# Optimization experiments

Measured on AMD Instinct MI355X. Metric: run time of the kernel, lower is better.

Reference implementation:

```python
import jax, jax.numpy as jnp
import numpy as np

N_NODES = 50000
N_EDGES = 1600000
IN_DIM = 64
HEADS = 8
DHEAD = 8  # out_dim per head
CLAMP = 5.0


def _xavier(key, shape):
    # xavier_normal_ for a torch Linear weight [out, in]; we store transposed [in, out]
    fan_in, fan_out = shape[0], shape[1]
    std = np.sqrt(2.0 / (fan_in + fan_out))
    return jax.random.normal(key, shape, jnp.float32) * jnp.float32(std)


def setup_inputs() -> dict:
    key = jax.random.key(0)
    ks = jax.random.split(key, 8)
    x = jax.random.normal(ks[0], (N_NODES, IN_DIM), jnp.float32)
    edge_attr = jax.random.normal(ks[1], (N_EDGES, IN_DIM), jnp.float32)
    edge_index = jax.random.randint(ks[2], (2, N_EDGES), 0, N_NODES)
    HD = HEADS * DHEAD
    WQ = _xavier(ks[3], (IN_DIM, HD)); bQ = jnp.zeros((HD,), jnp.float32)
    WK = _xavier(ks[4], (IN_DIM, HD))  # use_bias=False -> no bias for K
    WV = _xavier(ks[5], (IN_DIM, HD))  # no bias for V
    WE1 = _xavier(ks[6], (IN_DIM, HD)); bE1 = jnp.zeros((HD,), jnp.float32)
    return {"x": x, "edge_attr": edge_attr, "WQ": WQ, "bQ": bQ, "WK": WK,
            "WV": WV, "WE1": WE1, "bE1": bE1, "edge_index": edge_index}


def _segment_softmax(s, seg, num_segments):
    # pyg_softmax: numerically-stable softmax over edges grouped by destination node
    m = jax.ops.segment_max(s, seg, num_segments=num_segments)
    m = jnp.where(jnp.isfinite(m), m, jnp.float32(0.0))  # empty segments -> 0
    e = jnp.exp(s - m[seg])
    den = jax.ops.segment_sum(e, seg, num_segments=num_segments)
    return e / (den[seg] + jnp.float32(1e-16))


def _forward(x, edge_attr, WQ, bQ, WK, WV, WE1, bE1, edge_index):
    Q = (x @ WQ + bQ).reshape(N_NODES, HEADS, DHEAD)
    K = (x @ WK).reshape(N_NODES, HEADS, DHEAD)
    V = (x @ WV).reshape(N_NODES, HEADS, DHEAD)
    E = (edge_attr @ WE1 + bE1).reshape(N_EDGES, HEADS, DHEAD)
    src, dst = edge_index[0], edge_index[1]
    # score = K[src] * Q[dst]; score_e = score * E  (attn_product='mul', act=Identity)
    score_e = K[src] * Q[dst] * E                  # [Ne, H, D]
    wE = score_e.reshape(N_EDGES, HEADS * DHEAD)   # edge output
    s = score_e.sum(-1, keepdims=True) / jnp.sqrt(jnp.float32(DHEAD))  # [Ne, H, 1]
    s = jnp.clip(s, -CLAMP, CLAMP)
    alpha = _segment_softmax(s, dst, N_NODES)      # [Ne, H, 1]
    msg = V[src] * alpha
    wV = jax.ops.segment_sum(msg, dst, num_segments=N_NODES)
    # edge_enhance (edge_reweight=False): add segment-sum of score_e * alpha
    wV = wV + jax.ops.segment_sum(score_e * alpha, dst, num_segments=N_NODES)
    return wV, wE


def reference(x, edge_attr, WQ, bQ, WK, WV, WE1, bE1, edge_index):
    return _forward(x, edge_attr, WQ, bQ, WK, WV, WE1, bE1, edge_index)
```

## Files before the change

### kernel.cpp

```cpp
#include <hip/hip_runtime.h>

#define NN 50000
#define NE 1600000
#define CLAMP_V 5.0f
#define NB 2048
#define CH ((NE + NB - 1) / NB)
#define BSHIFT 9
#define NBUCK ((NN + (1 << BSHIFT) - 1) >> BSHIFT)
#define BPAD 128

typedef __attribute__((ext_vector_type(4))) short bf16x4;
typedef __attribute__((ext_vector_type(4))) float f32x4;

static __device__ __forceinline__ short f2bf(float x) {
    unsigned u = __builtin_bit_cast(unsigned, x);
    u += 0x7FFF + ((u >> 16) & 1);
    return (short)(u >> 16);
}

__global__ __launch_bounds__(256) void proj_kernel(
    const float* __restrict__ x,
    const float* __restrict__ WQ, const float* __restrict__ bQ,
    const float* __restrict__ WK, const float* __restrict__ WVw,
    float* __restrict__ Q, float* __restrict__ K, float* __restrict__ V)
{
    __shared__ float sWQ[4096], sWK[4096], sWV[4096];
    for (int i = threadIdx.x; i < 4096; i += 256) {
        sWQ[i] = WQ[i]; sWK[i] = WK[i]; sWV[i] = WVw[i];
    }
    __syncthreads();
    const int col = threadIdx.x & 63;
    const int nl  = threadIdx.x >> 6;
    const float bq = bQ[col];
    for (int node = blockIdx.x * 4 + nl; node < NN; node += gridDim.x * 4) {
        const float* xr = x + (size_t)node * 64;
        float aq = 0.f, ak = 0.f, av = 0.f;
        #pragma unroll
        for (int j = 0; j < 64; ++j) {
            float xv = xr[j];
            aq = fmaf(xv, sWQ[j*64+col], aq);
            ak = fmaf(xv, sWK[j*64+col], ak);
            av = fmaf(xv, sWV[j*64+col], av);
        }
        Q[(size_t)node*64+col] = aq + bq;
        K[(size_t)node*64+col] = ak;
        V[(size_t)node*64+col] = av;
    }
}

__global__ __launch_bounds__(256) void hist1_kernel(
    const int* __restrict__ ei, int* __restrict__ blockHist)
{
    __shared__ int h[BPAD];
    if (threadIdx.x < BPAD) h[threadIdx.x] = 0;
    __syncthreads();
    const int b  = blockIdx.x;
    const int e0 = b * CH;
    const int e1 = (e0 + CH < NE) ? e0 + CH : NE;
    for (int e = e0 + threadIdx.x; e < e1; e += 256)
        atomicAdd(&h[ei[NE + e] >> BSHIFT], 1);
    __syncthreads();
    if (threadIdx.x < NBUCK) blockHist[b * BPAD + threadIdx.x] = h[threadIdx.x];
}

__global__ __launch_bounds__(64) void scanA_kernel(
    int* __restrict__ blockHist, int* __restrict__ bucketTotal)
{
    const int k    = blockIdx.x;
    const int lane = threadIdx.x;
    int running = 0;
    for (int c = 0; c < NB; c += 64) {
        int v = blockHist[(c + lane) * BPAD + k];
        int incl = v;
        #pragma unroll
        for (int d = 1; d < 64; d <<= 1) {
            int t = __shfl_up(incl, d);
            if (lane >= d) incl += t;
        }
        blockHist[(c + lane) * BPAD + k] = running + (incl - v);
        running += __shfl(incl, 63);
    }
    if (lane == 0) bucketTotal[k] = running;
}

__global__ void scanB_kernel(const int* __restrict__ bucketTotal,
                             int* __restrict__ bucketStart)
{
    int acc = 0;
    for (int k = 0; k < NBUCK; ++k) { bucketStart[k] = acc; acc += bucketTotal[k]; }
    bucketStart[NBUCK] = acc;
}

__global__ __launch_bounds__(256) void scatter1_kernel(
    const int* __restrict__ ei, const int* __restrict__ blockHist,
    const int* __restrict__ bucketStart, uint2* __restrict__ binned)
{
    __shared__ int cur[BPAD];
    const int b = blockIdx.x;
    if (threadIdx.x < NBUCK)
        cur[threadIdx.x] = bucketStart[threadIdx.x] + blockHist[b * BPAD + threadIdx.x];
    __syncthreads();
    const int e0 = b * CH;
    const int e1 = (e0 + CH < NE) ? e0 + CH : NE;
    for (int e = e0 + threadIdx.x; e < e1; e += 256) {
        const unsigned src = ei[e], dst = ei[NE + e];
        const int pos = atomicAdd(&cur[dst >> BSHIFT], 1);
        binned[pos] = make_uint2((dst << 16) | src, (unsigned)e);
    }
}

__global__ __launch_bounds__(1024) void sort2_kernel(
    const uint2* __restrict__ binned, const int* __restrict__ bucketStart,
    uint2* __restrict__ sorted)
{
    __shared__ int cnt[512];
    __shared__ int pre[512];
    const int b  = blockIdx.x;
    const int lo = bucketStart[b];
    const int hi = bucketStart[b + 1];
    if (threadIdx.x < 512) cnt[threadIdx.x] = 0;
    __syncthreads();
    for (int p = lo + threadIdx.x; p < hi; p += 1024)
        atomicAdd(&cnt[(binned[p].x >> 16) & 511], 1);
    __syncthreads();
    if (threadIdx.x < 512) pre[threadIdx.x] = cnt[threadIdx.x];
    __syncthreads();
    for (int d = 1; d < 512; d <<= 1) {
        int t = (threadIdx.x < 512 && threadIdx.x >= d) ? pre[threadIdx.x - d] : 0;
        __syncthreads();
        if (threadIdx.x < 512) pre[threadIdx.x] += t;
        __syncthreads();
    }
    if (threadIdx.x < 512)
        cnt[threadIdx.x] = lo + pre[threadIdx.x] - cnt[threadIdx.x];
    __syncthreads();
    for (int p = lo + threadIdx.x; p < hi; p += 1024) {
        const uint2 q = binned[p];
        const int pos = atomicAdd(&cnt[(q.x >> 16) & 511], 1);
        sorted[pos] = q;
    }
}

__global__ __launch_bounds__(256) void edge_fused_kernel(
    const float* __restrict__ edge_attr,
    const float* __restrict__ WE1, const float* __restrict__ bE1,
    const uint2* __restrict__ sorted,
    const float* __restrict__ Q, const float* __restrict__ K,
    const float* __restrict__ V,
    float* __restrict__ wE, float* __restrict__ den, float* __restrict__ Num)
{
    __shared__ float Elds[4][16 * 64];
    __shared__ float exL[4][16 * 8];
    __shared__ int   dstL[4][16];
    const int tid  = threadIdx.x;
    const int wv   = tid >> 6;
    const int lane = tid & 63;
    const int g    = lane >> 4;
    const int rowl = lane & 15;

    bf16x4 bF[4][4];
    float  bias[4];
    #pragma unroll
    for (int cb = 0; cb < 4; ++cb) {
        const int col = rowl + 16 * cb;
        bias[cb] = bE1[col];
        #pragma unroll
        for (int ks = 0; ks < 4; ++ks) {
            bf16x4 t;
            #pragma unroll
            for (int j = 0; j < 4; ++j)
                t[j] = f2bf(WE1[(ks * 16 + g * 4 + j) * 64 + col]);
            bF[cb][ks] = t;
        }
    }

    const float inv_sqrt8 = 0.35355339059327373f;

    for (int tile = blockIdx.x; tile < (NE / 64); tile += gridDim.x) {
        const int pBase = tile * 64 + wv * 16;

        const uint2 qv  = sorted[pBase + rowl];
        const int  srcv = qv.x & 0xffff;
        const int  dstv = qv.x >> 16;
        const int  eidv = (int)qv.y;
        if (lane < 16) dstL[wv][lane] = dstv;

        bf16x4 aF[4];
        const float* ar = edge_attr + (size_t)eidv * 64 + g * 4;
        #pragma unroll
        for (int ks = 0; ks < 4; ++ks) {
            f32x4 v = __builtin_nontemporal_load(
                reinterpret_cast<const f32x4*>(ar + ks * 16));
            bf16x4 t;
            #pragma unroll
            for (int j = 0; j < 4; ++j) t[j] = f2bf(v[j]);
            aF[ks] = t;
        }

        f32x4 acc[4];
        #pragma unroll
        for (int cb = 0; cb < 4; ++cb) {
            acc[cb][0] = bias[cb]; acc[cb][1] = bias[cb];
            acc[cb][2] = bias[cb]; acc[cb][3] = bias[cb];
        }
        #pragma unroll
        for (int cb = 0; cb < 4; ++cb)
            #pragma unroll
            for (int ks = 0; ks < 4; ++ks)
                acc[cb] = __builtin_amdgcn_mfma_f32_16x16x16bf16_1k(
                    aF[ks], bF[cb][ks], acc[cb], 0, 0, 0);

        #pragma unroll
        for (int cb = 0; cb < 4; ++cb)
            #pragma unroll
            for (int r = 0; r < 4; ++r)
                Elds[wv][(g * 4 + r) * 64 + rowl + 16 * cb] = acc[cb][r];

        #pragma unroll
        for (int qi = 0; qi < 4; ++qi) {
            const int el  = qi * 4 + g;
            const int eid = __shfl(eidv, el);
            const int src = __shfl(srcv, el);
            const int dst = __shfl(dstv, el);
            const f32x4 Kv = *reinterpret_cast<const f32x4*>(K + (size_t)src * 64 + rowl * 4);
            const f32x4 Qv = *reinterpret_cast<const f32x4*>(Q + (size_t)dst * 64 + rowl * 4);
            const f32x4 Vv = *reinterpret_cast<const f32x4*>(V + (size_t)src * 64 + rowl * 4);
            f32x4* eslot = reinterpret_cast<f32x4*>(&Elds[wv][el * 64 + rowl * 4]);
            const f32x4 El = *eslot;
            f32x4 sc;
            #pragma unroll
            for (int j = 0; j < 4; ++j) sc[j] = Kv[j] * Qv[j] * El[j];
            __builtin_nontemporal_store(sc,
                reinterpret_cast<f32x4*>(wE + (size_t)eid * 64 + rowl * 4));
            float ss = sc[0] + sc[1] + sc[2] + sc[3];
            ss += __shfl_xor(ss, 1);
            float s = fminf(fmaxf(ss * inv_sqrt8, -CLAMP_V), CLAMP_V);
            float ex = __expf(s);
            if ((rowl & 1) == 0)
                exL[wv][el * 8 + (rowl >> 1)] = ex;
            f32x4 t;
            #pragma unroll
            for (int j = 0; j < 4; ++j) t[j] = ex * (Vv[j] + sc[j]);
            *eslot = t;
        }

        float accP = 0.f, accD = 0.f;
        int cur = dstL[wv][0];
        #pragma unroll
        for (int el = 0; el < 16; ++el) {
            accP += Elds[wv][el * 64 + lane];
            accD += exL[wv][el * 8 + (lane & 7)];
            const int nxt = (el < 15) ? dstL[wv][el + 1] : -1;
            if (nxt != cur) {
                atomicAdd(&Num[(size_t)cur * 64 + lane], accP);
                if (lane < 8) atomicAdd(&den[cur * 8 + lane], accD);
                accP = 0.f; accD = 0.f; cur = nxt;
            }
        }
    }
}

__global__ __launch_bounds__(256) void finalize_kernel(
    const float* __restrict__ Num, const float* __restrict__ den,
    float* __restrict__ wV)
{
    const int i = blockIdx.x * 256 + threadIdx.x;
    if (i >= NN * 16) return;
    const int c4 = i & 15;
    const int n  = i >> 4;
    const int h  = c4 >> 1;
    const float d = den[n * 8 + h] + 1e-16f;
    f32x4 v = reinterpret_cast<const f32x4*>(Num)[i];
    v[0] /= d; v[1] /= d; v[2] /= d; v[3] /= d;
    reinterpret_cast<f32x4*>(wV)[i] = v;
}

extern "C" void kernel_launch(void* const* d_in, const int* in_sizes, int n_in,
                              void* d_out, int out_size, void* d_ws, size_t ws_size,
                              hipStream_t stream) {
    const float* x         = (const float*)d_in[0];
    const float* edge_attr = (const float*)d_in[1];
    const float* WQ        = (const float*)d_in[2];
    const float* bQ        = (const float*)d_in[3];
    const float* WK        = (const float*)d_in[4];
    const float* WVw       = (const float*)d_in[5];
    const float* WE1       = (const float*)d_in[6];
    const float* bE1       = (const float*)d_in[7];
    const int*   ei        = (const int*)d_in[8];

    float* out = (float*)d_out;
    float* wV = out;
    float* wE = out + (size_t)NN * 64;

    float* Q           = (float*)d_ws;
    float* K           = Q + (size_t)NN * 64;
    float* V           = K + (size_t)NN * 64;
    float* den         = V + (size_t)NN * 64;
    float* Num         = den + (size_t)NN * 8;
    int*   blockHist   = (int*)(Num + (size_t)NN * 64);
    int*   bucketTotal = blockHist + NB * BPAD;
    int*   bucketStart = bucketTotal + BPAD;
    uint2* binned      = (uint2*)(bucketStart + BPAD);
    uint2* sorted      = binned + NE;

    hipMemsetAsync(den, 0, (size_t)NN * (8 + 64) * sizeof(float), stream);

    hist1_kernel<<<NB, 256, 0, stream>>>(ei, blockHist);
    scanA_kernel<<<NBUCK, 64, 0, stream>>>(blockHist, bucketTotal);
    scanB_kernel<<<1, 1, 0, stream>>>(bucketTotal, bucketStart);
    scatter1_kernel<<<NB, 256, 0, stream>>>(ei, blockHist, bucketStart, binned);
    sort2_kernel<<<NBUCK, 1024, 0, stream>>>(binned, bucketStart, sorted);
    proj_kernel<<<1024, 256, 0, stream>>>(x, WQ, bQ, WK, WVw, Q, K, V);
    edge_fused_kernel<<<2048, 256, 0, stream>>>(edge_attr, WE1, bE1, sorted,
                                                Q, K, V, wE, den, Num);
    finalize_kernel<<<(NN * 16 + 255) / 256, 256, 0, stream>>>(Num, den, wV);
}
```

Baseline: 354.5 us.

## Fuse histogram with projection, parallelize bucket scan, pad edge LDS, double edge grid

The histogram and node-projection kernels are merged into one launch, with block ranges split by blockIdx, which removes a launch and lets the two independent phases overlap. The single-thread bucket scan becomes a 64-lane wavefront shuffle scan. The edge kernel's LDS tile stride is padded from 64 to 68 to reduce bank conflicts, and its grid is doubled to 4096 blocks. The fused kernel always allocates 48KB of LDS even for histogram blocks, which may limit occupancy for that phase.

Result: slower. 402.1 us (+13.4%).

```diff
diff --git a/kernel.cpp b/kernel.cpp
--- a/kernel.cpp
+++ b/kernel.cpp
@@ -8,6 +8,8 @@
 #define BSHIFT 9
 #define NBUCK ((NN + (1 << BSHIFT) - 1) >> BSHIFT)
 #define BPAD 128
+#define PROJ_BLOCKS 1024
+#define ESTR 68
 
 typedef __attribute__((ext_vector_type(4))) short bf16x4;
 typedef __attribute__((ext_vector_type(4))) float f32x4;
@@ -18,13 +20,30 @@
     return (short)(u >> 16);
 }
 
-__global__ __launch_bounds__(256) void proj_kernel(
+__global__ __launch_bounds__(256) void histproj_kernel(
+    const int* __restrict__ ei, int* __restrict__ blockHist,
     const float* __restrict__ x,
     const float* __restrict__ WQ, const float* __restrict__ bQ,
     const float* __restrict__ WK, const float* __restrict__ WVw,
     float* __restrict__ Q, float* __restrict__ K, float* __restrict__ V)
 {
-    __shared__ float sWQ[4096], sWK[4096], sWV[4096];
+    __shared__ float sW[3 * 4096];
+    if (blockIdx.x < NB) {
+        int* h = (int*)sW;
+        if (threadIdx.x < BPAD) h[threadIdx.x] = 0;
+        __syncthreads();
+        const int b  = blockIdx.x;
+        const int e0 = b * CH;
+        const int e1 = (e0 + CH < NE) ? e0 + CH : NE;
+        for (int e = e0 + threadIdx.x; e < e1; e += 256)
+            atomicAdd(&h[ei[NE + e] >> BSHIFT], 1);
+        __syncthreads();
+        if (threadIdx.x < NBUCK) blockHist[b * BPAD + threadIdx.x] = h[threadIdx.x];
+        return;
+    }
+    float* sWQ = sW;
+    float* sWK = sW + 4096;
+    float* sWV = sW + 8192;
     for (int i = threadIdx.x; i < 4096; i += 256) {
         sWQ[i] = WQ[i]; sWK[i] = WK[i]; sWV[i] = WVw[i];
     }
@@ -32,7 +51,8 @@
     const int col = threadIdx.x & 63;
     const int nl  = threadIdx.x >> 6;
     const float bq = bQ[col];
-    for (int node = blockIdx.x * 4 + nl; node < NN; node += gridDim.x * 4) {
+    const int pb  = blockIdx.x - NB;
+    for (int node = pb * 4 + nl; node < NN; node += PROJ_BLOCKS * 4) {
         const float* xr = x + (size_t)node * 64;
         float aq = 0.f, ak = 0.f, av = 0.f;
         #pragma unroll
@@ -46,21 +66,6 @@
         K[(size_t)node*64+col] = ak;
         V[(size_t)node*64+col] = av;
     }
-}
-
-__global__ __launch_bounds__(256) void hist1_kernel(
-    const int* __restrict__ ei, int* __restrict__ blockHist)
-{
-    __shared__ int h[BPAD];
-    if (threadIdx.x < BPAD) h[threadIdx.x] = 0;
-    __syncthreads();
-    const int b  = blockIdx.x;
-    const int e0 = b * CH;
-    const int e1 = (e0 + CH < NE) ? e0 + CH : NE;
-    for (int e = e0 + threadIdx.x; e < e1; e += 256)
-        atomicAdd(&h[ei[NE + e] >> BSHIFT], 1);
-    __syncthreads();
-    if (threadIdx.x < NBUCK) blockHist[b * BPAD + threadIdx.x] = h[threadIdx.x];
 }
 
 __global__ __launch_bounds__(64) void scanA_kernel(
@@ -83,12 +88,23 @@
     if (lane == 0) bucketTotal[k] = running;
 }
 
-__global__ void scanB_kernel(const int* __restrict__ bucketTotal,
-                             int* __restrict__ bucketStart)
-{
-    int acc = 0;
-    for (int k = 0; k < NBUCK; ++k) { bucketStart[k] = acc; acc += bucketTotal[k]; }
-    bucketStart[NBUCK] = acc;
+__global__ __launch_bounds__(64) void scanB_kernel(
+    const int* __restrict__ bucketTotal, int* __restrict__ bucketStart)
+{
+    const int lane = threadIdx.x;
+    int carry = 0;
+    for (int base = 0; base <= NBUCK; base += 64) {
+        const int idx = base + lane;
+        int v = (idx < NBUCK) ? bucketTotal[idx] : 0;
+        int incl = v;
+        #pragma unroll
+        for (int d = 1; d < 64; d <<= 1) {
+            int t = __shfl_up(incl, d);
+            if (lane >= d) incl += t;
+        }
+        if (idx <= NBUCK) bucketStart[idx] = carry + incl - v;
+        carry += __shfl(incl, 63);
+    }
 }
 
 __global__ __launch_bounds__(256) void scatter1_kernel(
@@ -149,7 +165,7 @@
     const float* __restrict__ V,
     float* __restrict__ wE, float* __restrict__ den, float* __restrict__ Num)
 {
-    __shared__ float Elds[4][16 * 64];
+    __shared__ float Elds[4][16 * ESTR];
     __shared__ float exL[4][16 * 8];
     __shared__ int   dstL[4][16];
     const int tid  = threadIdx.x;
@@ -214,7 +230,7 @@
         for (int cb = 0; cb < 4; ++cb)
             #pragma unroll
             for (int r = 0; r < 4; ++r)
-                Elds[wv][(g * 4 + r) * 64 + rowl + 16 * cb] = acc[cb][r];
+                Elds[wv][(g * 4 + r) * ESTR + rowl + 16 * cb] = acc[cb][r];
 
         #pragma unroll
         for (int qi = 0; qi < 4; ++qi) {
@@ -225,7 +241,7 @@
             const f32x4 Kv = *reinterpret_cast<const f32x4*>(K + (size_t)src * 64 + rowl * 4);
             const f32x4 Qv = *reinterpret_cast<const f32x4*>(Q + (size_t)dst * 64 + rowl * 4);
             const f32x4 Vv = *reinterpret_cast<const f32x4*>(V + (size_t)src * 64 + rowl * 4);
-            f32x4* eslot = reinterpret_cast<f32x4*>(&Elds[wv][el * 64 + rowl * 4]);
+            f32x4* eslot = reinterpret_cast<f32x4*>(&Elds[wv][el * ESTR + rowl * 4]);
             const f32x4 El = *eslot;
             f32x4 sc;
             #pragma unroll
@@ -248,7 +264,7 @@
         int cur = dstL[wv][0];
         #pragma unroll
         for (int el = 0; el < 16; ++el) {
-            accP += Elds[wv][el * 64 + lane];
+            accP += Elds[wv][el * ESTR + lane];
             accD += exL[wv][el * 8 + (lane & 7)];
             const int nxt = (el < 15) ? dstL[wv][el + 1] : -1;
             if (nxt != cur) {
@@ -305,13 +321,13 @@
 
     hipMemsetAsync(den, 0, (size_t)NN * (8 + 64) * sizeof(float), stream);
 
-    hist1_kernel<<<NB, 256, 0, stream>>>(ei, blockHist);
+    histproj_kernel<<<NB + PROJ_BLOCKS, 256, 0, stream>>>(
+        ei, blockHist, x, WQ, bQ, WK, WVw, Q, K, V);
     scanA_kernel<<<NBUCK, 64, 0, stream>>>(blockHist, bucketTotal);
-    scanB_kernel<<<1, 1, 0, stream>>>(bucketTotal, bucketStart);
+    scanB_kernel<<<1, 64, 0, stream>>>(bucketTotal, bucketStart);
     scatter1_kernel<<<NB, 256, 0, stream>>>(ei, blockHist, bucketStart, binned);
     sort2_kernel<<<NBUCK, 1024, 0, stream>>>(binned, bucketStart, sorted);
-    proj_kernel<<<1024, 256, 0, stream>>>(x, WQ, bQ, WK, WVw, Q, K, V);
-    edge_fused_kernel<<<2048, 256, 0, stream>>>(edge_attr, WE1, bE1, sorted,
+    edge_fused_kernel<<<4096, 256, 0, stream>>>(edge_attr, WE1, bE1, sorted,
                                                 Q, K, V, wE, den, Num);
     finalize_kernel<<<(NN * 16 + 255) / 256, 256, 0, stream>>>(Num, den, wV);
 }
```
